# Performance work log

Hardware: AMD Instinct MI355X
Metric: run time of the kernel (lower is better)

## Reference

```python
import jax, jax.numpy as jnp
import numpy as np

N_NODES = 100000
N_EDGES = 1600000
IN_C, HID_C, OUT_C, K = 128, 128, 64, 3


def setup_inputs() -> dict:
    key = jax.random.key(0)
    ks = jax.random.split(key, 8)
    x = jax.random.normal(ks[0], (N_NODES, IN_C), dtype=jnp.float32)
    edge_index = jax.random.randint(ks[1], (2, N_EDGES), 0, N_NODES, dtype=jnp.int64)
    s = 0.05
    W0 = jax.random.normal(ks[2], (K, IN_C, HID_C), dtype=jnp.float32) * s
    b0 = jnp.zeros((HID_C,), dtype=jnp.float32)
    W1 = jax.random.normal(ks[3], (K, HID_C, HID_C), dtype=jnp.float32) * s
    b1 = jnp.zeros((HID_C,), dtype=jnp.float32)
    W2 = jax.random.normal(ks[4], (K, HID_C, OUT_C), dtype=jnp.float32) * s
    b2 = jnp.zeros((OUT_C,), dtype=jnp.float32)
    return {"x": x, "edge_index": edge_index, "W0": W0, "b0": b0,
            "W1": W1, "b1": b1, "W2": W2, "b2": b2}


def reference(x, edge_index, W0, b0, W1, b1, W2, b2):
    # PyG ChebConv with normalization='sym', lambda_max=2.0:
    # L_hat = L - I = -D^{-1/2} A D^{-1/2}  (self-loop weight nets to zero)
    src, dst = edge_index[0], edge_index[1]
    n = x.shape[0]
    deg = jax.ops.segment_sum(jnp.ones(src.shape, x.dtype), src, num_segments=n)
    dinv = jnp.where(deg > 0, jax.lax.rsqrt(deg), 0.0)
    w = -dinv[src] * dinv[dst]  # [E] edge weights of L_hat

    def prop(h):  # y[dst] += w * h[src]  (sparse L_hat @ h)
        return jax.ops.segment_sum(w[:, None] * h[src], dst, num_segments=n)

    def cheb_conv(h, W, b):
        # Tx_0 = h; Tx_1 = L_hat h; Tx_k = 2 L_hat Tx_{k-1} - Tx_{k-2}
        Tx0 = h
        out = Tx0 @ W[0]
        Tx1 = prop(Tx0)
        out = out + Tx1 @ W[1]
        for k in range(2, W.shape[0]):
            Tx2 = 2.0 * prop(Tx1) - Tx0
            out = out + Tx2 @ W[k]
            Tx0, Tx1 = Tx1, Tx2
        return out + b

    h = jax.nn.relu(cheb_conv(x, W0, b0))   # dropout is identity in eval mode
    h = jax.nn.relu(cheb_conv(h, W1, b1))
    return cheb_conv(h, W2, b2)
```

## Files before the change

### kernel.cpp

```cpp
#include <hip/hip_runtime.h>
#include <hip/hip_bf16.h>

#define NN 100000
#define NE 1600000
#define NB 196
#define BSH 9
#define SCH 4096

typedef _Float16 f16;
typedef __attribute__((ext_vector_type(2))) _Float16 h2;
typedef __attribute__((ext_vector_type(8))) _Float16 f16x8;
typedef __attribute__((ext_vector_type(8))) short short8;
typedef __attribute__((ext_vector_type(4))) float f32x4;

__device__ __forceinline__ short f16b(float x) {
    f16 h = (f16)x; short s; __builtin_memcpy(&s, &h, 2); return s;
}
__device__ __forceinline__ int h2i(h2 v) { int r; __builtin_memcpy(&r, &v, 4); return r; }
__device__ __forceinline__ h2 i2h(int v) { h2 r; __builtin_memcpy(&r, &v, 4); return r; }

__global__ __launch_bounds__(256) void hist_kernel(const int* __restrict__ src,
                                                   const int* __restrict__ dst,
                                                   int* __restrict__ binS,
                                                   int* __restrict__ binD, int E) {
    __shared__ int hS[NB], hD[NB];
    for (int i = threadIdx.x; i < NB; i += 256) { hS[i] = 0; hD[i] = 0; }
    __syncthreads();
    for (int e = blockIdx.x * 256 + threadIdx.x; e < E; e += gridDim.x * 256) {
        atomicAdd(&hS[src[e] >> BSH], 1);
        atomicAdd(&hD[dst[e] >> BSH], 1);
    }
    __syncthreads();
    for (int i = threadIdx.x; i < NB; i += 256) {
        if (hS[i]) atomicAdd(&binS[i], hS[i]);
        if (hD[i]) atomicAdd(&binD[i], hD[i]);
    }
}

__global__ void scan_kernel(const int* __restrict__ binS, const int* __restrict__ binD,
                            int* __restrict__ curS, int* __restrict__ offS,
                            int* __restrict__ curD, int* __restrict__ offD,
                            int* __restrict__ rowptr, int E) {
    if (threadIdx.x == 0 && blockIdx.x == 0) {
        int rs = 0, rd = 0;
        for (int i = 0; i < NB; ++i) {
            curS[i] = rs; offS[i] = rs; rs += binS[i];
            curD[i] = rd; offD[i] = rd; rd += binD[i];
        }
        offS[NB] = rs;
        offD[NB] = rd;
        rowptr[NN] = E;
    }
}

__global__ __launch_bounds__(256) void scatter_kernel(const int* __restrict__ src,
                                                      const int* __restrict__ dst,
                                                      int* __restrict__ curS,
                                                      int* __restrict__ curD,
                                                      int* __restrict__ srcB,
                                                      int* __restrict__ packB, int E) {
    __shared__ int cS[NB], cD[NB], bS[NB], bD[NB];
    int base = blockIdx.x * SCH;
    for (int i = threadIdx.x; i < NB; i += 256) { cS[i] = 0; cD[i] = 0; }
    __syncthreads();
    int s[16], d[16], rS[16], rD[16];
#pragma unroll
    for (int k = 0; k < 16; ++k) {
        int idx = base + k * 256 + threadIdx.x;
        if (idx < E) {
            s[k] = src[idx]; d[k] = dst[idx];
            rS[k] = atomicAdd(&cS[s[k] >> BSH], 1);
            rD[k] = atomicAdd(&cD[d[k] >> BSH], 1);
        } else {
            s[k] = -1;
        }
    }
    __syncthreads();
    for (int i = threadIdx.x; i < NB; i += 256) {
        if (cS[i]) bS[i] = atomicAdd(&curS[i], cS[i]);
        if (cD[i]) bD[i] = atomicAdd(&curD[i], cD[i]);
    }
    __syncthreads();
#pragma unroll
    for (int k = 0; k < 16; ++k) {
        if (s[k] >= 0) {
            srcB[bS[s[k] >> BSH] + rS[k]] = s[k];
            packB[bD[d[k] >> BSH] + rD[k]] = s[k] | ((d[k] & 511) << 20);
        }
    }
}

__global__ __launch_bounds__(256) void csr_kernel(const int* __restrict__ offD,
                                                  const int* __restrict__ packB,
                                                  int* __restrict__ rowptr,
                                                  int* __restrict__ csrCol, int n) {
    int b = blockIdx.x;
    int node0 = b << BSH;
    int nNodes = min(512, n - node0);
    if (nNodes <= 0) return;
    int beg = offD[b], end = offD[b + 1];
    __shared__ int h[512];
    __shared__ int roff[512];
    for (int i = threadIdx.x; i < 512; i += 256) h[i] = 0;
    __syncthreads();
    for (int p = beg + threadIdx.x; p < end; p += 256)
        atomicAdd(&h[(packB[p] >> 20) & 511], 1);
    __syncthreads();
    if (threadIdx.x == 0) {
        int r = beg;
        for (int i = 0; i < 512; ++i) { roff[i] = r; r += h[i]; }
    }
    __syncthreads();
    for (int i = threadIdx.x; i < nNodes; i += 256) rowptr[node0 + i] = roff[i];
    for (int i = threadIdx.x; i < 512; i += 256) h[i] = 0;
    __syncthreads();
    for (int p = beg + threadIdx.x; p < end; p += 256) {
        int pk = packB[p];
        int dl = (pk >> 20) & 511;
        int r = atomicAdd(&h[dl], 1);
        csrCol[roff[dl] + r] = pk & 0xFFFFF;
    }
}

__global__ __launch_bounds__(256) void deg_kernel(const int* __restrict__ offS,
                                                  const int* __restrict__ srcB,
                                                  float* __restrict__ dinv, int n) {
    int b = blockIdx.x;
    int node0 = b << BSH;
    int nNodes = min(512, n - node0);
    if (nNodes <= 0) return;
    int beg = offS[b], end = offS[b + 1];
    __shared__ int h[512];
    for (int i = threadIdx.x; i < 512; i += 256) h[i] = 0;
    __syncthreads();
    for (int p = beg + threadIdx.x; p < end; p += 256)
        atomicAdd(&h[srcB[p] & 511], 1);
    __syncthreads();
    for (int i = threadIdx.x; i < nNodes; i += 256) {
        int d = h[i];
        dinv[node0 + i] = d > 0 ? rsqrtf((float)d) : 0.0f;
    }
}

__global__ void convw_kernel(const float* __restrict__ W0, const float* __restrict__ W1,
                             const float* __restrict__ W2, short* __restrict__ Bt0,
                             short* __restrict__ Bt1, short* __restrict__ Bt2) {
    int i = blockIdx.x * blockDim.x + threadIdx.x;
    if (i < 49152) {
        int j = i >> 7, k = i & 127;
        int t = j >> 7, o = j & 127;
        float v = (t == 0) ? W0[k * 128 + o] - W0[2 * 16384 + k * 128 + o]
                : (t == 1) ? W0[16384 + k * 128 + o]
                           : 2.f * W0[2 * 16384 + k * 128 + o];
        Bt0[j * 128 + k] = f16b(v);
    } else if (i < 98304) {
        int m = i - 49152;
        int j = m >> 7, k = m & 127;
        int t = j >> 7, o = j & 127;
        float v = (t == 0) ? W1[k * 128 + o] - W1[2 * 16384 + k * 128 + o]
                : (t == 1) ? W1[16384 + k * 128 + o]
                           : 2.f * W1[2 * 16384 + k * 128 + o];
        Bt1[j * 128 + k] = f16b(v);
    } else if (i < 122880) {
        int m = i - 98304;
        int j = m >> 7, k = m & 127;
        int t = j >> 6, o = j & 63;
        float v = (t == 0) ? W2[k * 64 + o] - W2[2 * 8192 + k * 64 + o]
                : (t == 1) ? W2[8192 + k * 64 + o]
                           : 2.f * W2[2 * 8192 + k * 64 + o];
        Bt2[j * 128 + k] = f16b(v);
    }
}

__global__ __launch_bounds__(256) void copyx_kernel(const float* __restrict__ x,
                                                    short* __restrict__ xb, int n) {
    int i = blockIdx.x * 256 + threadIdx.x;
    if (i < n * 16) {
        const float4* xp = (const float4*)x + (size_t)i * 2;
        float4 f0 = xp[0], f1 = xp[1];
        short8 v;
        v[0] = f16b(f0.x); v[1] = f16b(f0.y); v[2] = f16b(f0.z); v[3] = f16b(f0.w);
        v[4] = f16b(f1.x); v[5] = f16b(f1.y); v[6] = f16b(f1.z); v[7] = f16b(f1.w);
        *(short8*)(xb + (size_t)i * 8) = v;
    }
}

template <int C>
__global__ __launch_bounds__(256) void gemm_kernel(const short* __restrict__ A,
                                                   const short* __restrict__ Bt,
                                                   const float* __restrict__ bias,
                                                   short* out0, short* out1, short* out2,
                                                   int n) {
    constexpr int BNT = 3 * C;
    constexpr int WC = BNT / 96;
    constexpr int WR = 4 / WC;
    constexpr int WM = 64 / WR;
    constexpr int MF = WM / 16;
    constexpr int NF = 6;
    constexpr int LDP = 40;
    constexpr int BSLOT = BNT * 4;
    constexpr int BITER = BSLOT / 256;
    __shared__ short lds[(64 + BNT) * LDP];
    short* As = lds;
    short* Bs = lds + 64 * LDP;

    int tid = threadIdx.x;
    int lane = tid & 63;
    int wid = tid >> 6;
    int wy = wid / WC;
    int wx = wid % WC;
    int row0 = blockIdx.x * 64;
    int l15 = lane & 15;
    int kb = (lane >> 4) * 8;

    int ar = tid >> 2, aseg = tid & 3;
    int agr = row0 + ar;

    f32x4 acc[MF][NF];
#pragma unroll
    for (int i = 0; i < MF; ++i)
#pragma unroll
        for (int j = 0; j < NF; ++j) acc[i][j] = (f32x4){0.f, 0.f, 0.f, 0.f};

    for (int step = 0; step < 4; ++step) {
        int k0 = step * 32;
        short8 va = (agr < n)
            ? *(const short8*)(A + (size_t)agr * 128 + k0 + aseg * 8)
            : (short8){0, 0, 0, 0, 0, 0, 0, 0};
        *(short8*)&As[ar * LDP + aseg * 8] = va;
#pragma unroll
        for (int i = 0; i < BITER; ++i) {
            int slot = tid + i * 256;
            int j = slot >> 2, seg = slot & 3;
            *(short8*)&Bs[j * LDP + seg * 8] =
                *(const short8*)(Bt + (size_t)j * 128 + k0 + seg * 8);
        }
        __syncthreads();
        f16x8 af[MF], bfr[NF];
#pragma unroll
        for (int mf = 0; mf < MF; ++mf)
            af[mf] = *(f16x8*)&As[(wy * WM + mf * 16 + l15) * LDP + kb];
#pragma unroll
        for (int nf = 0; nf < NF; ++nf)
            bfr[nf] = *(f16x8*)&Bs[(wx * 96 + nf * 16 + l15) * LDP + kb];
#pragma unroll
        for (int mf = 0; mf < MF; ++mf)
#pragma unroll
            for (int nf = 0; nf < NF; ++nf)
                acc[mf][nf] = __builtin_amdgcn_mfma_f32_16x16x32_f16(
                    af[mf], bfr[nf], acc[mf][nf], 0, 0, 0);
        __syncthreads();
    }

    float bb[NF];
#pragma unroll
    for (int nf = 0; nf < NF; ++nf) {
        int colc = wx * 96 + nf * 16 + l15;
        bb[nf] = (colc < C) ? bias[colc] : 0.f;
    }
    short* st = lds + wid * 1536;
#pragma unroll
    for (int mf = 0; mf < MF; ++mf) {
#pragma unroll
        for (int nf = 0; nf < NF; ++nf) {
#pragma unroll
            for (int r = 0; r < 4; ++r) {
                int fr = (lane >> 4) * 4 + r;
                st[fr * 96 + nf * 16 + l15] = f16b(acc[mf][nf][r] + bb[nf]);
            }
        }
#pragma unroll
        for (int u = 0; u < 3; ++u) {
            int unit = u * 64 + lane;
            int rr = unit / 12;
            int seg = unit - rr * 12;
            int grow = row0 + wy * WM + mf * 16 + rr;
            int colc = wx * 96 + seg * 8;
            int t = colc / C, off = colc - t * C;
            short* P = (t == 0) ? out0 : (t == 1) ? out1 : out2;
            if (grow < n)
                *(int4*)&P[(size_t)grow * C + off] = *(const int4*)&st[rr * 96 + seg * 8];
        }
    }
}

template <int C, int RELU, int OUTF>
__global__ __launch_bounds__(256) void prop_kernel(const short* __restrict__ G,
                                                   const short* __restrict__ Add,
                                                   void* __restrict__ O,
                                                   const int* __restrict__ rowptr,
                                                   const int* __restrict__ csrCol,
                                                   const float* __restrict__ dinv, int n) {
    constexpr int LPE = C / 8;
    constexpr int EPG = 64 / LPE;
    constexpr int STEP = 4 * EPG;
    int wid = (blockIdx.x * blockDim.x + threadIdx.x) >> 6;
    int lane = threadIdx.x & 63;
    if (wid >= n) return;
    int beg = rowptr[wid];
    int c = rowptr[wid + 1] - beg;
    int sg = lane / LPE;
    int sl = lane & (LPE - 1);
    h2 a0 = {0, 0}, a1 = {0, 0}, a2 = {0, 0}, a3 = {0, 0};
    for (int b0 = 0; b0 < c; b0 += 64) {
        int cb = min(64, c - b0);
        int myc = 0, mywp = 0;
        if (lane < cb) {
            myc = csrCol[beg + b0 + lane];
            f16 hw = (f16)dinv[myc];
            h2 p = {hw, hw};
            mywp = h2i(p);
        }
        for (int base = 0; base < cb; base += STEP) {
            int j0 = base + sg, j1 = j0 + EPG, j2 = j0 + 2 * EPG, j3 = j0 + 3 * EPG;
            int s0 = __shfl(myc, j0);  int w0 = __shfl(mywp, j0);
            int s1 = __shfl(myc, j1);  int w1 = __shfl(mywp, j1);
            int s2 = __shfl(myc, j2);  int w2 = __shfl(mywp, j2);
            int s3 = __shfl(myc, j3);  int w3 = __shfl(mywp, j3);
            int4 v0 = *(const int4*)(G + (size_t)s0 * C + sl * 8);
            int4 v1 = *(const int4*)(G + (size_t)s1 * C + sl * 8);
            int4 v2 = *(const int4*)(G + (size_t)s2 * C + sl * 8);
            int4 v3 = *(const int4*)(G + (size_t)s3 * C + sl * 8);
            h2 p0 = i2h(w0), p1 = i2h(w1), p2 = i2h(w2), p3 = i2h(w3);
            a0 = i2h(v0.x) * p0 + a0; a1 = i2h(v0.y) * p0 + a1;
            a2 = i2h(v0.z) * p0 + a2; a3 = i2h(v0.w) * p0 + a3;
            a0 = i2h(v1.x) * p1 + a0; a1 = i2h(v1.y) * p1 + a1;
            a2 = i2h(v1.z) * p1 + a2; a3 = i2h(v1.w) * p1 + a3;
            a0 = i2h(v2.x) * p2 + a0; a1 = i2h(v2.y) * p2 + a1;
            a2 = i2h(v2.z) * p2 + a2; a3 = i2h(v2.w) * p2 + a3;
            a0 = i2h(v3.x) * p3 + a0; a1 = i2h(v3.y) * p3 + a1;
            a2 = i2h(v3.z) * p3 + a2; a3 = i2h(v3.w) * p3 + a3;
        }
    }
#pragma unroll
    for (int off = LPE; off < 64; off <<= 1) {
        a0 += i2h(__shfl_xor(h2i(a0), off));
        a1 += i2h(__shfl_xor(h2i(a1), off));
        a2 += i2h(__shfl_xor(h2i(a2), off));
        a3 += i2h(__shfl_xor(h2i(a3), off));
    }
    if (lane < LPE) {
        float scale = -dinv[wid];
        int4 ad = *(const int4*)(Add + (size_t)wid * C + sl * 8);
        h2 d0 = i2h(ad.x), d1 = i2h(ad.y), d2 = i2h(ad.z), d3 = i2h(ad.w);
        float r0 = fmaf(scale, (float)a0[0], (float)d0[0]);
        float r1 = fmaf(scale, (float)a0[1], (float)d0[1]);
        float r2 = fmaf(scale, (float)a1[0], (float)d1[0]);
        float r3 = fmaf(scale, (float)a1[1], (float)d1[1]);
        float r4 = fmaf(scale, (float)a2[0], (float)d2[0]);
        float r5 = fmaf(scale, (float)a2[1], (float)d2[1]);
        float r6 = fmaf(scale, (float)a3[0], (float)d3[0]);
        float r7 = fmaf(scale, (float)a3[1], (float)d3[1]);
        if (RELU) {
            r0 = fmaxf(r0, 0.f); r1 = fmaxf(r1, 0.f); r2 = fmaxf(r2, 0.f);
            r3 = fmaxf(r3, 0.f); r4 = fmaxf(r4, 0.f); r5 = fmaxf(r5, 0.f);
            r6 = fmaxf(r6, 0.f); r7 = fmaxf(r7, 0.f);
        }
        if (OUTF) {
            float* op = (float*)O + (size_t)wid * C + sl * 8;
            *(float4*)op = make_float4(r0, r1, r2, r3);
            *(float4*)(op + 4) = make_float4(r4, r5, r6, r7);
        } else {
            int4 w;
            h2 o0 = {(f16)r0, (f16)r1}, o1 = {(f16)r2, (f16)r3};
            h2 o2 = {(f16)r4, (f16)r5}, o3 = {(f16)r6, (f16)r7};
            w.x = h2i(o0); w.y = h2i(o1); w.z = h2i(o2); w.w = h2i(o3);
            *(int4*)((short*)O + (size_t)wid * C + sl * 8) = w;
        }
    }
}

extern "C" void kernel_launch(void* const* d_in, const int* in_sizes, int n_in,
                              void* d_out, int out_size, void* d_ws, size_t ws_size,
                              hipStream_t stream) {
    const float* x  = (const float*)d_in[0];
    const int*   ei = (const int*)d_in[1];
    const float* W0 = (const float*)d_in[2];
    const float* b0 = (const float*)d_in[3];
    const float* W1 = (const float*)d_in[4];
    const float* b1 = (const float*)d_in[5];
    const float* W2 = (const float*)d_in[6];
    const float* b2 = (const float*)d_in[7];
    float* out = (float*)d_out;

    const int n = NN, E = NE;
    const int* src = ei;
    const int* dst = ei + E;

    char* ws = (char*)d_ws;
    auto alloc = [&](size_t bytes) -> void* {
        void* p = (void*)ws;
        ws += (bytes + 255) & ~(size_t)255;
        return p;
    };
    int*   binS   = (int*)alloc(NB * 4);
    int*   binD   = (int*)alloc(NB * 4);
    int*   curS   = (int*)alloc((NB + 1) * 4);
    int*   offS   = (int*)alloc((NB + 1) * 4);
    int*   curD   = (int*)alloc((NB + 1) * 4);
    int*   offD   = (int*)alloc((NB + 1) * 4);
    int*   srcB   = (int*)alloc((size_t)E * 4);
    int*   packB  = (int*)alloc((size_t)E * 4);
    int*   rowptr = (int*)alloc((size_t)(n + 1) * 4);
    int*   csrCol = (int*)alloc((size_t)E * 4);
    float* dinv   = (float*)alloc((size_t)n * 4);
    short* xb     = (short*)alloc((size_t)n * 128 * 2);
    short* buf0   = (short*)alloc((size_t)n * 128 * 2);
    short* buf1   = (short*)alloc((size_t)n * 128 * 2);
    short* buf2   = (short*)alloc((size_t)n * 128 * 2);
    short* buf3   = (short*)alloc((size_t)n * 128 * 2);
    short* Bt0    = (short*)alloc((size_t)384 * 128 * 2);
    short* Bt1    = (short*)alloc((size_t)384 * 128 * 2);
    short* Bt2    = (short*)alloc((size_t)192 * 128 * 2);

    hipMemsetAsync(binS, 0, NB * 4, stream);
    hipMemsetAsync(binD, 0, NB * 4, stream);

    const int TPB = 256;

    hist_kernel<<<256, TPB, 0, stream>>>(src, dst, binS, binD, E);
    scan_kernel<<<1, 64, 0, stream>>>(binS, binD, curS, offS, curD, offD, rowptr, E);
    int sChunks = (E + SCH - 1) / SCH;
    scatter_kernel<<<sChunks, TPB, 0, stream>>>(src, dst, curS, curD, srcB, packB, E);
    csr_kernel<<<NB, TPB, 0, stream>>>(offD, packB, rowptr, csrCol, n);
    deg_kernel<<<NB, TPB, 0, stream>>>(offS, srcB, dinv, n);

    convw_kernel<<<(122880 + 255) / 256, 256, 0, stream>>>(W0, W1, W2, Bt0, Bt1, Bt2);
    copyx_kernel<<<(n * 16 + 255) / 256, 256, 0, stream>>>(x, xb, n);

    int pBlocks = (n + 3) / 4;
    int gBlocks = (n + 63) / 64;

    gemm_kernel<128><<<gBlocks, 256, 0, stream>>>(xb, Bt0, b0, buf0, buf1, buf2, n);
    prop_kernel<128, 0, 0><<<pBlocks, 256, 0, stream>>>(buf2, buf1, buf3, rowptr, csrCol, dinv, n);
    prop_kernel<128, 1, 0><<<pBlocks, 256, 0, stream>>>(buf3, buf0, buf1, rowptr, csrCol, dinv, n);
    gemm_kernel<128><<<gBlocks, 256, 0, stream>>>(buf1, Bt1, b1, buf0, buf1, buf2, n);
    prop_kernel<128, 0, 0><<<pBlocks, 256, 0, stream>>>(buf2, buf1, buf3, rowptr, csrCol, dinv, n);
    prop_kernel<128, 1, 0><<<pBlocks, 256, 0, stream>>>(buf3, buf0, buf1, rowptr, csrCol, dinv, n);
    gemm_kernel<64><<<gBlocks, 256, 0, stream>>>(buf1, Bt2, b2, buf0, buf3, buf2, n);
    prop_kernel<64, 0, 0><<<pBlocks, 256, 0, stream>>>(buf2, buf3, buf0 + (size_t)n * 64,
                                                       rowptr, csrCol, dinv, n);
    prop_kernel<64, 0, 1><<<pBlocks, 256, 0, stream>>>(buf0 + (size_t)n * 64, buf0, out,
                                                       rowptr, csrCol, dinv, n);
}
```

Baseline: 518.5 us.

## Split 128-wide feature buffers into two 64-column slices mapped to XCD groups

```diff
diff --git a/kernel.cpp b/kernel.cpp
--- a/kernel.cpp
+++ b/kernel.cpp
@@ -176,12 +176,14 @@
                                                     short* __restrict__ xb, int n) {
     int i = blockIdx.x * 256 + threadIdx.x;
     if (i < n * 16) {
-        const float4* xp = (const float4*)x + (size_t)i * 2;
+        int row = i >> 4, ch8 = i & 15;
+        int c = ch8 * 8;
+        const float4* xp = (const float4*)(x + (size_t)row * 128 + c);
         float4 f0 = xp[0], f1 = xp[1];
         short8 v;
         v[0] = f16b(f0.x); v[1] = f16b(f0.y); v[2] = f16b(f0.z); v[3] = f16b(f0.w);
         v[4] = f16b(f1.x); v[5] = f16b(f1.y); v[6] = f16b(f1.z); v[7] = f16b(f1.w);
-        *(short8*)(xb + (size_t)i * 8) = v;
+        *(short8*)(xb + ((size_t)(c >> 6) * n + row) * 64 + (c & 63)) = v;
     }
 }
 
@@ -224,8 +226,9 @@
 
     for (int step = 0; step < 4; ++step) {
         int k0 = step * 32;
+        int c = k0 + aseg * 8;
         short8 va = (agr < n)
-            ? *(const short8*)(A + (size_t)agr * 128 + k0 + aseg * 8)
+            ? *(const short8*)(A + ((size_t)(c >> 6) * n + agr) * 64 + (c & 63))
             : (short8){0, 0, 0, 0, 0, 0, 0, 0};
         *(short8*)&As[ar * LDP + aseg * 8] = va;
 #pragma unroll
@@ -276,31 +279,38 @@
             int seg = unit - rr * 12;
             int grow = row0 + wy * WM + mf * 16 + rr;
             int colc = wx * 96 + seg * 8;
-            int t = colc / C, off = colc - t * C;
+            int t = colc / C, cc = colc - t * C;
             short* P = (t == 0) ? out0 : (t == 1) ? out1 : out2;
-            if (grow < n)
-                *(int4*)&P[(size_t)grow * C + off] = *(const int4*)&st[rr * 96 + seg * 8];
-        }
-    }
-}
-
-template <int C, int RELU, int OUTF>
-__global__ __launch_bounds__(256) void prop_kernel(const short* __restrict__ G,
-                                                   const short* __restrict__ Add,
-                                                   void* __restrict__ O,
-                                                   const int* __restrict__ rowptr,
-                                                   const int* __restrict__ csrCol,
-                                                   const float* __restrict__ dinv, int n) {
-    constexpr int LPE = C / 8;
-    constexpr int EPG = 64 / LPE;
-    constexpr int STEP = 4 * EPG;
-    int wid = (blockIdx.x * blockDim.x + threadIdx.x) >> 6;
+            if (grow < n) {
+                size_t addr = (C == 128)
+                    ? ((size_t)(cc >> 6) * n + grow) * 64 + (cc & 63)
+                    : (size_t)grow * 64 + cc;
+                *(int4*)&P[addr] = *(const int4*)&st[rr * 96 + seg * 8];
+            }
+        }
+    }
+}
+
+template <int RELU>
+__global__ __launch_bounds__(256) void propS_kernel(const short* __restrict__ G,
+                                                    const short* __restrict__ Add,
+                                                    short* __restrict__ O,
+                                                    const int* __restrict__ rowptr,
+                                                    const int* __restrict__ csrCol,
+                                                    const float* __restrict__ dinv, int n) {
+    int bid = blockIdx.x;
+    int xcd = bid & 7;
+    int slice = xcd >> 2;
+    int chunk = (bid >> 3) * 4 + (xcd & 3);
+    int wv = threadIdx.x >> 6;
     int lane = threadIdx.x & 63;
+    int wid = chunk * 4 + wv;
     if (wid >= n) return;
     int beg = rowptr[wid];
     int c = rowptr[wid + 1] - beg;
-    int sg = lane / LPE;
-    int sl = lane & (LPE - 1);
+    int sg = lane >> 3;
+    int sl = lane & 7;
+    const short* Gs = G + (size_t)slice * n * 64;
     h2 a0 = {0, 0}, a1 = {0, 0}, a2 = {0, 0}, a3 = {0, 0};
     for (int b0 = 0; b0 < c; b0 += 64) {
         int cb = min(64, c - b0);
@@ -311,16 +321,16 @@
             h2 p = {hw, hw};
             mywp = h2i(p);
         }
-        for (int base = 0; base < cb; base += STEP) {
-            int j0 = base + sg, j1 = j0 + EPG, j2 = j0 + 2 * EPG, j3 = j0 + 3 * EPG;
+        for (int base = 0; base < cb; base += 32) {
+            int j0 = base + sg, j1 = j0 + 8, j2 = j0 + 16, j3 = j0 + 24;
             int s0 = __shfl(myc, j0);  int w0 = __shfl(mywp, j0);
             int s1 = __shfl(myc, j1);  int w1 = __shfl(mywp, j1);
             int s2 = __shfl(myc, j2);  int w2 = __shfl(mywp, j2);
             int s3 = __shfl(myc, j3);  int w3 = __shfl(mywp, j3);
-            int4 v0 = *(const int4*)(G + (size_t)s0 * C + sl * 8);
-            int4 v1 = *(const int4*)(G + (size_t)s1 * C + sl * 8);
-            int4 v2 = *(const int4*)(G + (size_t)s2 * C + sl * 8);
-            int4 v3 = *(const int4*)(G + (size_t)s3 * C + sl * 8);
+            int4 v0 = *(const int4*)(Gs + (size_t)s0 * 64 + sl * 8);
+            int4 v1 = *(const int4*)(Gs + (size_t)s1 * 64 + sl * 8);
+            int4 v2 = *(const int4*)(Gs + (size_t)s2 * 64 + sl * 8);
+            int4 v3 = *(const int4*)(Gs + (size_t)s3 * 64 + sl * 8);
             h2 p0 = i2h(w0), p1 = i2h(w1), p2 = i2h(w2), p3 = i2h(w3);
             a0 = i2h(v0.x) * p0 + a0; a1 = i2h(v0.y) * p0 + a1;
             a2 = i2h(v0.z) * p0 + a2; a3 = i2h(v0.w) * p0 + a3;
@@ -333,15 +343,16 @@
         }
     }
 #pragma unroll
-    for (int off = LPE; off < 64; off <<= 1) {
+    for (int off = 8; off < 64; off <<= 1) {
         a0 += i2h(__shfl_xor(h2i(a0), off));
         a1 += i2h(__shfl_xor(h2i(a1), off));
         a2 += i2h(__shfl_xor(h2i(a2), off));
         a3 += i2h(__shfl_xor(h2i(a3), off));
     }
-    if (lane < LPE) {
+    if (lane < 8) {
         float scale = -dinv[wid];
-        int4 ad = *(const int4*)(Add + (size_t)wid * C + sl * 8);
+        size_t rb = ((size_t)slice * n + wid) * 64 + sl * 8;
+        int4 ad = *(const int4*)(Add + rb);
         h2 d0 = i2h(ad.x), d1 = i2h(ad.y), d2 = i2h(ad.z), d3 = i2h(ad.w);
         float r0 = fmaf(scale, (float)a0[0], (float)d0[0]);
         float r1 = fmaf(scale, (float)a0[1], (float)d0[1]);
@@ -356,8 +367,85 @@
             r3 = fmaxf(r3, 0.f); r4 = fmaxf(r4, 0.f); r5 = fmaxf(r5, 0.f);
             r6 = fmaxf(r6, 0.f); r7 = fmaxf(r7, 0.f);
         }
+        int4 w;
+        h2 o0 = {(f16)r0, (f16)r1}, o1 = {(f16)r2, (f16)r3};
+        h2 o2 = {(f16)r4, (f16)r5}, o3 = {(f16)r6, (f16)r7};
+        w.x = h2i(o0); w.y = h2i(o1); w.z = h2i(o2); w.w = h2i(o3);
+        *(int4*)(O + rb) = w;
+    }
+}
+
+template <int RELU, int OUTF>
+__global__ __launch_bounds__(256) void prop64_kernel(const short* __restrict__ G,
+                                                     const short* __restrict__ Add,
+                                                     void* __restrict__ O,
+                                                     const int* __restrict__ rowptr,
+                                                     const int* __restrict__ csrCol,
+                                                     const float* __restrict__ dinv, int n) {
+    int wid = (blockIdx.x * blockDim.x + threadIdx.x) >> 6;
+    int lane = threadIdx.x & 63;
+    if (wid >= n) return;
+    int beg = rowptr[wid];
+    int c = rowptr[wid + 1] - beg;
+    int sg = lane >> 3;
+    int sl = lane & 7;
+    h2 a0 = {0, 0}, a1 = {0, 0}, a2 = {0, 0}, a3 = {0, 0};
+    for (int b0 = 0; b0 < c; b0 += 64) {
+        int cb = min(64, c - b0);
+        int myc = 0, mywp = 0;
+        if (lane < cb) {
+            myc = csrCol[beg + b0 + lane];
+            f16 hw = (f16)dinv[myc];
+            h2 p = {hw, hw};
+            mywp = h2i(p);
+        }
+        for (int base = 0; base < cb; base += 32) {
+            int j0 = base + sg, j1 = j0 + 8, j2 = j0 + 16, j3 = j0 + 24;
+            int s0 = __shfl(myc, j0);  int w0 = __shfl(mywp, j0);
+            int s1 = __shfl(myc, j1);  int w1 = __shfl(mywp, j1);
+            int s2 = __shfl(myc, j2);  int w2 = __shfl(mywp, j2);
+            int s3 = __shfl(myc, j3);  int w3 = __shfl(mywp, j3);
+            int4 v0 = *(const int4*)(G + (size_t)s0 * 64 + sl * 8);
+            int4 v1 = *(const int4*)(G + (size_t)s1 * 64 + sl * 8);
+            int4 v2 = *(const int4*)(G + (size_t)s2 * 64 + sl * 8);
+            int4 v3 = *(const int4*)(G + (size_t)s3 * 64 + sl * 8);
+            h2 p0 = i2h(w0), p1 = i2h(w1), p2 = i2h(w2), p3 = i2h(w3);
+            a0 = i2h(v0.x) * p0 + a0; a1 = i2h(v0.y) * p0 + a1;
+            a2 = i2h(v0.z) * p0 + a2; a3 = i2h(v0.w) * p0 + a3;
+            a0 = i2h(v1.x) * p1 + a0; a1 = i2h(v1.y) * p1 + a1;
+            a2 = i2h(v1.z) * p1 + a2; a3 = i2h(v1.w) * p1 + a3;
+            a0 = i2h(v2.x) * p2 + a0; a1 = i2h(v2.y) * p2 + a1;
+            a2 = i2h(v2.z) * p2 + a2; a3 = i2h(v2.w) * p2 + a3;
+            a0 = i2h(v3.x) * p3 + a0; a1 = i2h(v3.y) * p3 + a1;
+            a2 = i2h(v3.z) * p3 + a2; a3 = i2h(v3.w) * p3 + a3;
+        }
+    }
+#pragma unroll
+    for (int off = 8; off < 64; off <<= 1) {
+        a0 += i2h(__shfl_xor(h2i(a0), off));
+        a1 += i2h(__shfl_xor(h2i(a1), off));
+        a2 += i2h(__shfl_xor(h2i(a2), off));
+        a3 += i2h(__shfl_xor(h2i(a3), off));
+    }
+    if (lane < 8) {
+        float scale = -dinv[wid];
+        int4 ad = *(const int4*)(Add + (size_t)wid * 64 + sl * 8);
+        h2 d0 = i2h(ad.x), d1 = i2h(ad.y), d2 = i2h(ad.z), d3 = i2h(ad.w);
+        float r0 = fmaf(scale, (float)a0[0], (float)d0[0]);
+        float r1 = fmaf(scale, (float)a0[1], (float)d0[1]);
+        float r2 = fmaf(scale, (float)a1[0], (float)d1[0]);
+        float r3 = fmaf(scale, (float)a1[1], (float)d1[1]);
+        float r4 = fmaf(scale, (float)a2[0], (float)d2[0]);
+        float r5 = fmaf(scale, (float)a2[1], (float)d2[1]);
+        float r6 = fmaf(scale, (float)a3[0], (float)d3[0]);
+        float r7 = fmaf(scale, (float)a3[1], (float)d3[1]);
+        if (RELU) {
+            r0 = fmaxf(r0, 0.f); r1 = fmaxf(r1, 0.f); r2 = fmaxf(r2, 0.f);
+            r3 = fmaxf(r3, 0.f); r4 = fmaxf(r4, 0.f); r5 = fmaxf(r5, 0.f);
+            r6 = fmaxf(r6, 0.f); r7 = fmaxf(r7, 0.f);
+        }
         if (OUTF) {
-            float* op = (float*)O + (size_t)wid * C + sl * 8;
+            float* op = (float*)O + (size_t)wid * 64 + sl * 8;
             *(float4*)op = make_float4(r0, r1, r2, r3);
             *(float4*)(op + 4) = make_float4(r4, r5, r6, r7);
         } else {
@@ -365,7 +453,7 @@
             h2 o0 = {(f16)r0, (f16)r1}, o1 = {(f16)r2, (f16)r3};
             h2 o2 = {(f16)r4, (f16)r5}, o3 = {(f16)r6, (f16)r7};
             w.x = h2i(o0); w.y = h2i(o1); w.z = h2i(o2); w.w = h2i(o3);
-            *(int4*)((short*)O + (size_t)wid * C + sl * 8) = w;
+            *(int4*)((short*)O + (size_t)wid * 64 + sl * 8) = w;
         }
     }
 }
@@ -428,18 +516,20 @@
     convw_kernel<<<(122880 + 255) / 256, 256, 0, stream>>>(W0, W1, W2, Bt0, Bt1, Bt2);
     copyx_kernel<<<(n * 16 + 255) / 256, 256, 0, stream>>>(x, xb, n);
 
-    int pBlocks = (n + 3) / 4;
     int gBlocks = (n + 63) / 64;
+    int chunksPerSlice = (n + 3) / 4;
+    int sBlocksP = ((chunksPerSlice + 3) / 4) * 8;
+    int pBlocks64 = (n + 3) / 4;
 
     gemm_kernel<128><<<gBlocks, 256, 0, stream>>>(xb, Bt0, b0, buf0, buf1, buf2, n);
-    prop_kernel<128, 0, 0><<<pBlocks, 256, 0, stream>>>(buf2, buf1, buf3, rowptr, csrCol, dinv, n);
-    prop_kernel<128, 1, 0><<<pBlocks, 256, 0, stream>>>(buf3, buf0, buf1, rowptr, csrCol, dinv, n);
+    propS_kernel<0><<<sBlocksP, 256, 0, stream>>>(buf2, buf1, buf3, rowptr, csrCol, dinv, n);
+    propS_kernel<1><<<sBlocksP, 256, 0, stream>>>(buf3, buf0, buf1, rowptr, csrCol, dinv, n);
     gemm_kernel<128><<<gBlocks, 256, 0, stream>>>(buf1, Bt1, b1, buf0, buf1, buf2, n);
-    prop_kernel<128, 0, 0><<<pBlocks, 256, 0, stream>>>(buf2, buf1, buf3, rowptr, csrCol, dinv, n);
-    prop_kernel<128, 1, 0><<<pBlocks, 256, 0, stream>>>(buf3, buf0, buf1, rowptr, csrCol, dinv, n);
+    propS_kernel<0><<<sBlocksP, 256, 0, stream>>>(buf2, buf1, buf3, rowptr, csrCol, dinv, n);
+    propS_kernel<1><<<sBlocksP, 256, 0, stream>>>(buf3, buf0, buf1, rowptr, csrCol, dinv, n);
     gemm_kernel<64><<<gBlocks, 256, 0, stream>>>(buf1, Bt2, b2, buf0, buf3, buf2, n);
-    prop_kernel<64, 0, 0><<<pBlocks, 256, 0, stream>>>(buf2, buf3, buf0 + (size_t)n * 64,
+    prop64_kernel<0, 0><<<pBlocks64, 256, 0, stream>>>(buf2, buf3, buf0 + (size_t)n * 64,
                                                        rowptr, csrCol, dinv, n);
-    prop_kernel<64, 0, 1><<<pBlocks, 256, 0, stream>>>(buf0 + (size_t)n * 64, buf0, out,
+    prop64_kernel<0, 1><<<pBlocks64, 256, 0, stream>>>(buf0 + (size_t)n * 64, buf0, out,
                                                        rowptr, csrCol, dinv, n);
 }
```

Measured after the change: 566.3 us. 1.09x slower.
